# Kernel tuning notes

Hardware: AMD Instinct MI355X
Metric: run time of the kernel (lower is better)

The kernel has to match this reference:

```python
import jax, jax.numpy as jnp
import numpy as np

B, H, N, D = 4, 16, 2048, 128  # batch, num_head, maxlen, head_dim (qkdim == vdim)
EPS = 1e-6


def _act(x):
    # '1+elu' kernel feature map
    return jax.nn.elu(x) + 1.0


def _simple_rms_norm(x):
    # SimpleRMSNorm over the last dim: x / sqrt(mean(x^2) + eps), no learned scale
    ms = jnp.mean(jnp.square(x), axis=-1, keepdims=True)
    return x * jax.lax.rsqrt(ms + EPS)


def setup_inputs() -> dict:
    key = jax.random.key(0)
    kq, kk, kv, km = jax.random.split(key, 4)
    Q = jax.random.normal(kq, (B, H, N, D), dtype=jnp.float32)
    K = jax.random.normal(kk, (B, H, N, D), dtype=jnp.float32)
    V = jax.random.normal(kv, (B, H, N, D), dtype=jnp.float32)
    mask = jax.random.uniform(km, (B, N), dtype=jnp.float32)
    return {"Q": Q, "K": K, "V": V, "mask": mask}


def reference(Q, K, V, mask):
    m = mask[:, None, :, None]           # (B, 1, N, 1)
    Qf = _act(Q)                          # (B, H, N, D)
    Kf = _act(K) * m                      # masked feature-mapped keys
    Vf = V * m                            # masked values
    # non-causal linear attention: KV = sum_n K_n (x) V_n ; out = Q @ KV
    KV = jnp.einsum('bhnd,bhne->bhde', Kf, Vf)    # (B, H, D, D)
    out = jnp.einsum('bhde,bhnd->bhne', KV, Qf)   # (B, H, N, D)
    return _simple_rms_norm(out)
```

## Files before the change

### kernel.cpp

```cpp
#include <hip/hip_runtime.h>
#include <hip/hip_bf16.h>

#define NB 4
#define NH 16
#define NBH 64
#define NSEQ 2048
#define DD 128
#define EPS 1e-6f

typedef __bf16 bf16x8 __attribute__((ext_vector_type(8)));
typedef __bf16 bf16x4 __attribute__((ext_vector_type(4)));
typedef float  f32x4  __attribute__((ext_vector_type(4)));

__device__ __forceinline__ float elu1(float x) {
    return x > 0.f ? x + 1.f : __expf(x);
}

__global__ __launch_bounds__(512) void kv_partial_kernel(
    const float* __restrict__ K, const float* __restrict__ V,
    const float* __restrict__ mask, float* __restrict__ part)
{
    __shared__ __bf16 KfT[128 * 72];
    __shared__ __bf16 VfT[128 * 72];
    __shared__ float  mloc[256];

    const int s  = blockIdx.x;
    const int bh = blockIdx.y;
    const int b  = bh >> 4;
    const int t  = threadIdx.x;
    const int n0 = s * 256;

    if (t < 256) mloc[t] = mask[b * NSEQ + n0 + t];

    const int d    = t & 127;
    const int qtr  = t >> 7;
    const int lane = t & 63;
    const int w    = t >> 6;
    const int quad = lane >> 4;
    const int col  = lane & 15;

    f32x4 acc[8];
    #pragma unroll
    for (int nt = 0; nt < 8; ++nt) acc[nt] = (f32x4){0.f, 0.f, 0.f, 0.f};

    const float* Kb = K + ((size_t)bh * NSEQ + n0) * DD;
    const float* Vb = V + ((size_t)bh * NSEQ + n0) * DD;

    for (int sub = 0; sub < 4; ++sub) {
        __syncthreads();
        #pragma unroll
        for (int r0 = 0; r0 < 16; r0 += 4) {
            bf16x4 kp, vp;
            #pragma unroll
            for (int j = 0; j < 4; ++j) {
                int nl = sub * 64 + qtr * 16 + r0 + j;
                float m  = mloc[nl];
                float kx = Kb[(size_t)nl * DD + d];
                float vx = Vb[(size_t)nl * DD + d];
                kp[j] = (__bf16)(elu1(kx) * m);
                vp[j] = (__bf16)(vx * m);
            }
            int nn = qtr * 16 + r0;
            *(bf16x4*)&KfT[d * 72 + nn] = kp;
            *(bf16x4*)&VfT[d * 72 + nn] = vp;
        }
        __syncthreads();

        #pragma unroll
        for (int kk = 0; kk < 2; ++kk) {
            int k0 = kk * 32 + quad * 8;
            bf16x8 a = *(bf16x8*)&VfT[(w * 16 + col) * 72 + k0];
            #pragma unroll
            for (int nt = 0; nt < 8; ++nt) {
                bf16x8 bb = *(bf16x8*)&KfT[(nt * 16 + col) * 72 + k0];
                acc[nt] = __builtin_amdgcn_mfma_f32_16x16x32_bf16(a, bb, acc[nt], 0, 0, 0);
            }
        }
    }

    float* po = part + (((size_t)bh * 8 + s) << 14);
    #pragma unroll
    for (int r = 0; r < 4; ++r) {
        int e = w * 16 + quad * 4 + r;
        #pragma unroll
        for (int nt = 0; nt < 8; ++nt)
            po[e * 128 + nt * 16 + col] = acc[nt][r];
    }
}

__global__ __launch_bounds__(256) void kv_reduce_kernel(
    const float* __restrict__ part, __bf16* __restrict__ kvt)
{
    int gid = blockIdx.x * 256 + threadIdx.x;
    int i   = gid * 4;
    int bh  = i >> 14;
    int ii  = i & 16383;
    const float* p = part + (((size_t)bh * 8) << 14) + ii;
    f32x4 sum = (f32x4){0.f, 0.f, 0.f, 0.f};
    #pragma unroll
    for (int s = 0; s < 8; ++s)
        sum += *(const f32x4*)(p + ((size_t)s << 14));
    bf16x4 o;
    o[0] = (__bf16)sum[0]; o[1] = (__bf16)sum[1];
    o[2] = (__bf16)sum[2]; o[3] = (__bf16)sum[3];
    *(bf16x4*)&kvt[i] = o;
}

__global__ __launch_bounds__(256) void qkv_norm_kernel(
    const float* __restrict__ Q, const __bf16* __restrict__ kvt,
    float* __restrict__ out)
{
    __shared__ __bf16 KVT[128 * 136];
    __shared__ __bf16 Qf[64 * 136];

    const int bh   = blockIdx.y;
    const int row0 = blockIdx.x * 64;
    const int t    = threadIdx.x;
    const int lane = t & 63;
    const int w    = t >> 6;
    const int quad = lane >> 4;
    const int col  = lane & 15;

    {
        const __bf16* src = kvt + ((size_t)bh << 14);
        #pragma unroll
        for (int i = 0; i < 8; ++i) {
            int idx = i * 256 + t;
            int e   = idx >> 4;
            int dd  = (idx & 15) * 8;
            *(bf16x8*)&KVT[e * 136 + dd] = *(const bf16x8*)&src[e * 128 + dd];
        }
    }
    {
        const float* Qb = Q + ((size_t)bh * NSEQ + row0) * DD;
        #pragma unroll
        for (int i = 0; i < 8; ++i) {
            int idx = i * 256 + t;
            int r   = idx >> 5;
            int dd  = (idx & 31) * 4;
            f32x4 q = *(const f32x4*)&Qb[r * DD + dd];
            bf16x4 qq;
            qq[0] = (__bf16)elu1(q[0]); qq[1] = (__bf16)elu1(q[1]);
            qq[2] = (__bf16)elu1(q[2]); qq[3] = (__bf16)elu1(q[3]);
            *(bf16x4*)&Qf[r * 136 + dd] = qq;
        }
    }
    __syncthreads();

    f32x4 acc[8];
    #pragma unroll
    for (int et = 0; et < 8; ++et) acc[et] = (f32x4){0.f, 0.f, 0.f, 0.f};

    #pragma unroll
    for (int kk = 0; kk < 4; ++kk) {
        int k0 = kk * 32 + quad * 8;
        bf16x8 a = *(bf16x8*)&Qf[(w * 16 + col) * 136 + k0];
        #pragma unroll
        for (int et = 0; et < 8; ++et) {
            bf16x8 bb = *(bf16x8*)&KVT[(et * 16 + col) * 136 + k0];
            acc[et] = __builtin_amdgcn_mfma_f32_16x16x32_bf16(a, bb, acc[et], 0, 0, 0);
        }
    }

    float* ob = out + ((size_t)bh * NSEQ + row0) * DD;
    #pragma unroll
    for (int r = 0; r < 4; ++r) {
        float p = 0.f;
        #pragma unroll
        for (int et = 0; et < 8; ++et) p += acc[et][r] * acc[et][r];
        p += __shfl_xor(p, 1);
        p += __shfl_xor(p, 2);
        p += __shfl_xor(p, 4);
        p += __shfl_xor(p, 8);
        float scale = rsqrtf(p * (1.0f / 128.0f) + EPS);
        int row = w * 16 + quad * 4 + r;
        #pragma unroll
        for (int et = 0; et < 8; ++et)
            ob[row * DD + et * 16 + col] = acc[et][r] * scale;
    }
}

extern "C" void kernel_launch(void* const* d_in, const int* in_sizes, int n_in,
                              void* d_out, int out_size, void* d_ws, size_t ws_size,
                              hipStream_t stream) {
    const float* Q    = (const float*)d_in[0];
    const float* K    = (const float*)d_in[1];
    const float* V    = (const float*)d_in[2];
    const float* mask = (const float*)d_in[3];
    float* out = (float*)d_out;

    float*  part = (float*)d_ws;
    __bf16* kvt  = (__bf16*)((char*)d_ws + (size_t)NBH * 8 * 16384 * 4);

    kv_partial_kernel<<<dim3(8, NBH), 512, 0, stream>>>(K, V, mask, part);
    kv_reduce_kernel<<<1024, 256, 0, stream>>>(part, kvt);
    qkv_norm_kernel<<<dim3(32, NBH), 256, 0, stream>>>(Q, kvt, out);
}
```

Before: 238.4 us.

## Retile KV partial and QKV kernels with 2x register tiles and bf16 partials

The KV partial kernel now uses 256 threads over 16 sequence chunks of 128 rows each. Each wave computes two 16-row output tiles so every K fragment is reused across two MFMAs, and K/V are loaded as vectorized float4. Partial sums are stored in bf16 instead of fp32, which halves workspace traffic and the reduce kernel's reads. The QKV kernel processes 128 rows per block with the same 2x register tiling to amortize the KV tile load. In exchange, rounding partials to bf16 before the 16-way sum costs some accuracy, and register pressure goes up.

```diff
diff --git a/kernel.cpp b/kernel.cpp
--- a/kernel.cpp
+++ b/kernel.cpp
@@ -1,12 +1,12 @@
 #include <hip/hip_runtime.h>
 #include <hip/hip_bf16.h>
 
-#define NB 4
-#define NH 16
 #define NBH 64
 #define NSEQ 2048
 #define DD 128
 #define EPS 1e-6f
+#define NCH 16
+#define CHROWS 128
 
 typedef __bf16 bf16x8 __attribute__((ext_vector_type(8)));
 typedef __bf16 bf16x4 __attribute__((ext_vector_type(4)));
@@ -16,105 +16,122 @@
     return x > 0.f ? x + 1.f : __expf(x);
 }
 
-__global__ __launch_bounds__(512) void kv_partial_kernel(
+__global__ __launch_bounds__(256, 3) void kv_partial_kernel(
     const float* __restrict__ K, const float* __restrict__ V,
-    const float* __restrict__ mask, float* __restrict__ part)
+    const float* __restrict__ mask, __bf16* __restrict__ part)
 {
     __shared__ __bf16 KfT[128 * 72];
     __shared__ __bf16 VfT[128 * 72];
-    __shared__ float  mloc[256];
+    __shared__ float  mloc[CHROWS];
 
     const int s  = blockIdx.x;
     const int bh = blockIdx.y;
     const int b  = bh >> 4;
     const int t  = threadIdx.x;
-    const int n0 = s * 256;
-
-    if (t < 256) mloc[t] = mask[b * NSEQ + n0 + t];
-
-    const int d    = t & 127;
-    const int qtr  = t >> 7;
+    const int n0 = s * CHROWS;
+
+    if (t < CHROWS) mloc[t] = mask[b * NSEQ + n0 + t];
+    __syncthreads();
+
+    const int rg   = t & 15;
+    const int d0   = (t >> 4) * 8;
     const int lane = t & 63;
     const int w    = t >> 6;
     const int quad = lane >> 4;
     const int col  = lane & 15;
 
-    f32x4 acc[8];
-    #pragma unroll
-    for (int nt = 0; nt < 8; ++nt) acc[nt] = (f32x4){0.f, 0.f, 0.f, 0.f};
+    f32x4 acc[2][8];
+    #pragma unroll
+    for (int i = 0; i < 2; ++i)
+        #pragma unroll
+        for (int dt = 0; dt < 8; ++dt) acc[i][dt] = (f32x4){0.f, 0.f, 0.f, 0.f};
 
     const float* Kb = K + ((size_t)bh * NSEQ + n0) * DD;
     const float* Vb = V + ((size_t)bh * NSEQ + n0) * DD;
 
-    for (int sub = 0; sub < 4; ++sub) {
+    #pragma unroll
+    for (int sub = 0; sub < 2; ++sub) {
+        bf16x4 kc[8], vc[8];
+        #pragma unroll
+        for (int j = 0; j < 4; ++j) {
+            const int nl = sub * 64 + rg * 4 + j;
+            const float m = mloc[nl];
+            f32x4 klo = *(const f32x4*)&Kb[(size_t)nl * DD + d0];
+            f32x4 khi = *(const f32x4*)&Kb[(size_t)nl * DD + d0 + 4];
+            f32x4 vlo = *(const f32x4*)&Vb[(size_t)nl * DD + d0];
+            f32x4 vhi = *(const f32x4*)&Vb[(size_t)nl * DD + d0 + 4];
+            #pragma unroll
+            for (int c = 0; c < 4; ++c) {
+                kc[c][j]     = (__bf16)(elu1(klo[c]) * m);
+                kc[4 + c][j] = (__bf16)(elu1(khi[c]) * m);
+                vc[c][j]     = (__bf16)(vlo[c] * m);
+                vc[4 + c][j] = (__bf16)(vhi[c] * m);
+            }
+        }
         __syncthreads();
         #pragma unroll
-        for (int r0 = 0; r0 < 16; r0 += 4) {
-            bf16x4 kp, vp;
-            #pragma unroll
-            for (int j = 0; j < 4; ++j) {
-                int nl = sub * 64 + qtr * 16 + r0 + j;
-                float m  = mloc[nl];
-                float kx = Kb[(size_t)nl * DD + d];
-                float vx = Vb[(size_t)nl * DD + d];
-                kp[j] = (__bf16)(elu1(kx) * m);
-                vp[j] = (__bf16)(vx * m);
+        for (int c = 0; c < 8; ++c) {
+            *(bf16x4*)&KfT[(d0 + c) * 72 + rg * 4] = kc[c];
+            *(bf16x4*)&VfT[(d0 + c) * 72 + rg * 4] = vc[c];
+        }
+        __syncthreads();
+        #pragma unroll
+        for (int kk = 0; kk < 2; ++kk) {
+            const int k0 = kk * 32 + quad * 8;
+            bf16x8 a0 = *(bf16x8*)&VfT[((2 * w)     * 16 + col) * 72 + k0];
+            bf16x8 a1 = *(bf16x8*)&VfT[((2 * w + 1) * 16 + col) * 72 + k0];
+            #pragma unroll
+            for (int dt = 0; dt < 8; ++dt) {
+                bf16x8 bb = *(bf16x8*)&KfT[(dt * 16 + col) * 72 + k0];
+                acc[0][dt] = __builtin_amdgcn_mfma_f32_16x16x32_bf16(a0, bb, acc[0][dt], 0, 0, 0);
+                acc[1][dt] = __builtin_amdgcn_mfma_f32_16x16x32_bf16(a1, bb, acc[1][dt], 0, 0, 0);
             }
-            int nn = qtr * 16 + r0;
-            *(bf16x4*)&KfT[d * 72 + nn] = kp;
-            *(bf16x4*)&VfT[d * 72 + nn] = vp;
-        }
-        __syncthreads();
-
-        #pragma unroll
-        for (int kk = 0; kk < 2; ++kk) {
-            int k0 = kk * 32 + quad * 8;
-            bf16x8 a = *(bf16x8*)&VfT[(w * 16 + col) * 72 + k0];
-            #pragma unroll
-            for (int nt = 0; nt < 8; ++nt) {
-                bf16x8 bb = *(bf16x8*)&KfT[(nt * 16 + col) * 72 + k0];
-                acc[nt] = __builtin_amdgcn_mfma_f32_16x16x32_bf16(a, bb, acc[nt], 0, 0, 0);
-            }
-        }
-    }
-
-    float* po = part + (((size_t)bh * 8 + s) << 14);
-    #pragma unroll
-    for (int r = 0; r < 4; ++r) {
-        int e = w * 16 + quad * 4 + r;
-        #pragma unroll
-        for (int nt = 0; nt < 8; ++nt)
-            po[e * 128 + nt * 16 + col] = acc[nt][r];
+        }
+    }
+
+    __bf16* po = part + ((size_t)(bh * NCH + s) << 14);
+    #pragma unroll
+    for (int i = 0; i < 2; ++i) {
+        #pragma unroll
+        for (int r = 0; r < 4; ++r) {
+            const int e = (2 * w + i) * 16 + quad * 4 + r;
+            #pragma unroll
+            for (int dt = 0; dt < 8; ++dt)
+                po[e * 128 + dt * 16 + col] = (__bf16)acc[i][dt][r];
+        }
     }
 }
 
 __global__ __launch_bounds__(256) void kv_reduce_kernel(
-    const float* __restrict__ part, __bf16* __restrict__ kvt)
+    const __bf16* __restrict__ part, __bf16* __restrict__ kvt)
 {
-    int gid = blockIdx.x * 256 + threadIdx.x;
-    int i   = gid * 4;
-    int bh  = i >> 14;
-    int ii  = i & 16383;
-    const float* p = part + (((size_t)bh * 8) << 14) + ii;
-    f32x4 sum = (f32x4){0.f, 0.f, 0.f, 0.f};
-    #pragma unroll
-    for (int s = 0; s < 8; ++s)
-        sum += *(const f32x4*)(p + ((size_t)s << 14));
-    bf16x4 o;
-    o[0] = (__bf16)sum[0]; o[1] = (__bf16)sum[1];
-    o[2] = (__bf16)sum[2]; o[3] = (__bf16)sum[3];
-    *(bf16x4*)&kvt[i] = o;
-}
-
-__global__ __launch_bounds__(256) void qkv_norm_kernel(
+    const int gid = blockIdx.x * 256 + threadIdx.x;
+    const int i   = gid * 8;
+    const int bh  = i >> 14;
+    const int ii  = i & 16383;
+    const __bf16* p = part + (((size_t)bh * NCH) << 14) + ii;
+    float sum[8] = {0.f, 0.f, 0.f, 0.f, 0.f, 0.f, 0.f, 0.f};
+    #pragma unroll
+    for (int s = 0; s < NCH; ++s) {
+        bf16x8 v = *(const bf16x8*)(p + ((size_t)s << 14));
+        #pragma unroll
+        for (int c = 0; c < 8; ++c) sum[c] += (float)v[c];
+    }
+    bf16x8 o;
+    #pragma unroll
+    for (int c = 0; c < 8; ++c) o[c] = (__bf16)sum[c];
+    *(bf16x8*)&kvt[i] = o;
+}
+
+__global__ __launch_bounds__(256, 2) void qkv_norm_kernel(
     const float* __restrict__ Q, const __bf16* __restrict__ kvt,
     float* __restrict__ out)
 {
     __shared__ __bf16 KVT[128 * 136];
-    __shared__ __bf16 Qf[64 * 136];
+    __shared__ __bf16 Qf[128 * 136];
 
     const int bh   = blockIdx.y;
-    const int row0 = blockIdx.x * 64;
+    const int row0 = blockIdx.x * 128;
     const int t    = threadIdx.x;
     const int lane = t & 63;
     const int w    = t >> 6;
@@ -125,58 +142,64 @@
         const __bf16* src = kvt + ((size_t)bh << 14);
         #pragma unroll
         for (int i = 0; i < 8; ++i) {
-            int idx = i * 256 + t;
-            int e   = idx >> 4;
-            int dd  = (idx & 15) * 8;
+            const int idx = i * 256 + t;
+            const int e   = idx >> 4;
+            const int dd  = (idx & 15) * 8;
             *(bf16x8*)&KVT[e * 136 + dd] = *(const bf16x8*)&src[e * 128 + dd];
         }
     }
     {
         const float* Qb = Q + ((size_t)bh * NSEQ + row0) * DD;
-        #pragma unroll
-        for (int i = 0; i < 8; ++i) {
-            int idx = i * 256 + t;
-            int r   = idx >> 5;
-            int dd  = (idx & 31) * 4;
-            f32x4 q = *(const f32x4*)&Qb[r * DD + dd];
+        const int qr  = t >> 1;
+        const int qd0 = (t & 1) * 64;
+        #pragma unroll
+        for (int j = 0; j < 16; ++j) {
+            f32x4 q = *(const f32x4*)&Qb[(size_t)qr * DD + qd0 + j * 4];
             bf16x4 qq;
             qq[0] = (__bf16)elu1(q[0]); qq[1] = (__bf16)elu1(q[1]);
             qq[2] = (__bf16)elu1(q[2]); qq[3] = (__bf16)elu1(q[3]);
-            *(bf16x4*)&Qf[r * 136 + dd] = qq;
+            *(bf16x4*)&Qf[qr * 136 + qd0 + j * 4] = qq;
         }
     }
     __syncthreads();
 
-    f32x4 acc[8];
-    #pragma unroll
-    for (int et = 0; et < 8; ++et) acc[et] = (f32x4){0.f, 0.f, 0.f, 0.f};
+    f32x4 acc[2][8];
+    #pragma unroll
+    for (int i = 0; i < 2; ++i)
+        #pragma unroll
+        for (int et = 0; et < 8; ++et) acc[i][et] = (f32x4){0.f, 0.f, 0.f, 0.f};
 
     #pragma unroll
     for (int kk = 0; kk < 4; ++kk) {
-        int k0 = kk * 32 + quad * 8;
-        bf16x8 a = *(bf16x8*)&Qf[(w * 16 + col) * 136 + k0];
+        const int k0 = kk * 32 + quad * 8;
+        bf16x8 a0 = *(bf16x8*)&Qf[((2 * w)     * 16 + col) * 136 + k0];
+        bf16x8 a1 = *(bf16x8*)&Qf[((2 * w + 1) * 16 + col) * 136 + k0];
         #pragma unroll
         for (int et = 0; et < 8; ++et) {
             bf16x8 bb = *(bf16x8*)&KVT[(et * 16 + col) * 136 + k0];
-            acc[et] = __builtin_amdgcn_mfma_f32_16x16x32_bf16(a, bb, acc[et], 0, 0, 0);
+            acc[0][et] = __builtin_amdgcn_mfma_f32_16x16x32_bf16(a0, bb, acc[0][et], 0, 0, 0);
+            acc[1][et] = __builtin_amdgcn_mfma_f32_16x16x32_bf16(a1, bb, acc[1][et], 0, 0, 0);
         }
     }
 
     float* ob = out + ((size_t)bh * NSEQ + row0) * DD;
     #pragma unroll
-    for (int r = 0; r < 4; ++r) {
-        float p = 0.f;
-        #pragma unroll
-        for (int et = 0; et < 8; ++et) p += acc[et][r] * acc[et][r];
-        p += __shfl_xor(p, 1);
-        p += __shfl_xor(p, 2);
-        p += __shfl_xor(p, 4);
-        p += __shfl_xor(p, 8);
-        float scale = rsqrtf(p * (1.0f / 128.0f) + EPS);
-        int row = w * 16 + quad * 4 + r;
-        #pragma unroll
-        for (int et = 0; et < 8; ++et)
-            ob[row * DD + et * 16 + col] = acc[et][r] * scale;
+    for (int i = 0; i < 2; ++i) {
+        #pragma unroll
+        for (int r = 0; r < 4; ++r) {
+            float p = 0.f;
+            #pragma unroll
+            for (int et = 0; et < 8; ++et) p += acc[i][et][r] * acc[i][et][r];
+            p += __shfl_xor(p, 1);
+            p += __shfl_xor(p, 2);
+            p += __shfl_xor(p, 4);
+            p += __shfl_xor(p, 8);
+            const float scale = rsqrtf(p * (1.0f / 128.0f) + EPS);
+            const int row = (2 * w + i) * 16 + quad * 4 + r;
+            #pragma unroll
+            for (int et = 0; et < 8; ++et)
+                ob[row * DD + et * 16 + col] = acc[i][et][r] * scale;
+        }
     }
 }
 
@@ -189,10 +212,10 @@
     const float* mask = (const float*)d_in[3];
     float* out = (float*)d_out;
 
-    float*  part = (float*)d_ws;
-    __bf16* kvt  = (__bf16*)((char*)d_ws + (size_t)NBH * 8 * 16384 * 4);
-
-    kv_partial_kernel<<<dim3(8, NBH), 512, 0, stream>>>(K, V, mask, part);
-    kv_reduce_kernel<<<1024, 256, 0, stream>>>(part, kvt);
-    qkv_norm_kernel<<<dim3(32, NBH), 256, 0, stream>>>(Q, kvt, out);
-}
+    __bf16* part = (__bf16*)d_ws;
+    __bf16* kvt  = part + (size_t)NBH * NCH * 16384;
+
+    kv_partial_kernel<<<dim3(NCH, NBH), 256, 0, stream>>>(K, V, mask, part);
+    kv_reduce_kernel<<<512, 256, 0, stream>>>(part, kvt);
+    qkv_norm_kernel<<<dim3(16, NBH), 256, 0, stream>>>(Q, kvt, out);
+}
```

Result: slower. 244.8 us (+2.6%).
